# Performance work log

Measured on AMD Instinct MI355X. Metric: run time of the kernel, lower is better.

## Reference

```python
import jax, jax.numpy as jnp
import numpy as np
import math

# static config
NH, HD, HID = 16, 128, 2048
ROT = 64            # head_dim * partial_rotary_factor(0.5)
EPS = 1e-6
GROUPS = 8
CHUNK = 64
THETA = 10000.0
LAYER_IDX, N_LAYERS = 1, 32
B, S = 2, 2048


def _base_slopes(n):
    # power-of-two branch of HF ALiBi slopes
    start = 2 ** (-(2 ** (-(math.log2(n) - 3))))
    return [start * (start ** i) for i in range(n)]

# per-head log-decay (negative): slope = -base * (1 - (l-1)/(L-1) + 1e-5)
SLOPE = jnp.asarray(
    -np.array(_base_slopes(NH), dtype=np.float32)
    * (1.0 - (LAYER_IDX - 1) / (N_LAYERS - 1) + 1e-5),
    dtype=jnp.float32)  # [NH]


def _rmsnorm(x, w):
    return x * jax.lax.rsqrt(jnp.mean(x * x, axis=-1, keepdims=True) + EPS) * w


def _partial_rope(x, positions):
    # x: [B,S,NH,HD]; neox-style rotary on first ROT dims, rest passthrough
    half = ROT // 2
    inv_freq = 1.0 / (THETA ** (jnp.arange(half, dtype=jnp.float32) / half))
    ang = positions.astype(jnp.float32)[:, None] * inv_freq       # [S, half]
    cos = jnp.cos(ang)[None, :, None, :]
    sin = jnp.sin(ang)[None, :, None, :]
    x1, x2, rest = x[..., :half], x[..., half:ROT], x[..., ROT:]
    return jnp.concatenate(
        [x1 * cos - x2 * sin, x2 * cos + x1 * sin, rest], axis=-1)


def setup_inputs() -> dict:
    key = jax.random.key(0)
    ks = jax.random.split(key, 4)
    return {
        'positions': jnp.arange(S, dtype=jnp.int32),
        'hidden_states': jax.random.normal(ks[0], (B, S, HID), jnp.float32),
        'recurrent_state': jnp.zeros((B, NH, HD, HD), jnp.float32),
        'w_qkv': jax.random.normal(ks[1], (HID, 3 * NH * HD), jnp.float32) * 0.02,
        'w_g': jax.random.normal(ks[2], (HID, NH * HD), jnp.float32) * 0.02,
        'w_dense': jax.random.normal(ks[3], (NH * HD, HID), jnp.float32) * 0.02,
        'q_norm_w': jnp.ones((HD,), jnp.float32),
        'k_norm_w': jnp.ones((HD,), jnp.float32),
        'g_norm_w': jnp.ones((NH * HD,), jnp.float32),
    }


def reference(positions, hidden_states, recurrent_state, w_qkv, w_g, w_dense,
              q_norm_w, k_norm_w, g_norm_w):
    # fused QKV projection
    qkv = hidden_states @ w_qkv                       # [B,S,3*NH*HD]
    q, k, v = jnp.split(qkv, 3, axis=-1)
    q = q.reshape(B, S, NH, HD)
    k = k.reshape(B, S, NH, HD)
    v = v.reshape(B, S, NH, HD)

    # QK RMSNorm then partial rotary
    q = _partial_rope(_rmsnorm(q, q_norm_w), positions)
    k = _partial_rope(_rmsnorm(k, k_norm_w), positions)

    # chunked ALiBi-decayed linear attention:
    #   S_t = lam * S_{t-1} + k_t v_t^T ; o_t = q_t S_t, lam = exp(slope)
    NC = S // CHUNK
    qc = q.reshape(B, NC, CHUNK, NH, HD).transpose(1, 0, 3, 2, 4)  # [NC,B,NH,C,HD]
    kc = k.reshape(B, NC, CHUNK, NH, HD).transpose(1, 0, 3, 2, 4)
    vc = v.reshape(B, NC, CHUNK, NH, HD).transpose(1, 0, 3, 2, 4)

    t = jnp.arange(CHUNK, dtype=jnp.float32)
    # intra-chunk causal decay mask lam^(i-j), i>=j: [NH,C,C]
    dec_mask = jnp.where(t[:, None] >= t[None, :],
                         jnp.exp(SLOPE[:, None, None] * (t[:, None] - t[None, :])),
                         0.0)
    q_dec = jnp.exp(SLOPE[:, None] * (t[None, :] + 1.0))            # [NH,C] lam^(i+1)
    k_dec = jnp.exp(SLOPE[:, None] * (CHUNK - 1.0 - t[None, :]))    # [NH,C] lam^(C-1-j)
    lam_C = jnp.exp(SLOPE * CHUNK)                                   # [NH]

    def step(state, inp):
        qb, kb, vb = inp                                  # [B,NH,C,HD]
        scores = jnp.einsum('bhid,bhjd->bhij', qb, kb) * dec_mask[None]
        o_intra = jnp.einsum('bhij,bhjd->bhid', scores, vb)
        o_inter = jnp.einsum('bhid,bhde->bhie', qb * q_dec[None, :, :, None], state)
        new_state = (state * lam_C[None, :, None, None]
                     + jnp.einsum('bhjd,bhje->bhde', kb * k_dec[None, :, :, None], vb))
        return new_state, o_intra + o_inter

    _, o = jax.lax.scan(step, recurrent_state, (qc, kc, vc))  # o: [NC,B,NH,C,HD]
    o = o.transpose(1, 0, 3, 2, 4).reshape(B, S, NH * HD)

    # GroupRMSNorm on attention output, sigmoid gate, output projection
    og = o.reshape(B, S, GROUPS, (NH * HD) // GROUPS)
    og = og * jax.lax.rsqrt(jnp.mean(og * og, axis=-1, keepdims=True) + EPS)
    o = og.reshape(B, S, NH * HD) * g_norm_w
    o = o * jax.nn.sigmoid(hidden_states @ w_g)
    return o @ w_dense
```

## Files before the change

kernel.cpp:

```cpp
#include <hip/hip_runtime.h>
#include <hip/hip_bf16.h>
#include <math.h>

#define NH   16
#define HD   128
#define HID  2048
#define NKV  6144
#define B_   2
#define S_   2048
#define NC   32
#define CHUNK_ 64
#define GROUPS_ 8

typedef __bf16 bf16_t;
typedef bf16_t bf16x8 __attribute__((ext_vector_type(8)));
typedef float  f32x4  __attribute__((ext_vector_type(4)));

__device__ __forceinline__ float b2f(unsigned int u) {
    union { unsigned int u; float f; } c; c.u = (u & 0xffffu) << 16; return c.f;
}
__device__ __forceinline__ unsigned int f2b(float f) {
    union { float f; unsigned int u; } c; c.f = f;
    unsigned int u = c.u;
    return (u + 0x7fffu + ((u >> 16) & 1u)) >> 16;
}

#define GLOAD_LDS16(gp, lp) __builtin_amdgcn_global_load_lds(                     \
    (const __attribute__((address_space(1))) void*)(gp),                          \
    (__attribute__((address_space(3))) void*)(lp), 16, 0, 0)

#define BAR()     asm volatile("s_barrier" ::: "memory")
#define VMCNT0()  asm volatile("s_waitcnt vmcnt(0)" ::: "memory")

__global__ __launch_bounds__(256) void cvt_bf16(const float* __restrict__ in,
                                                unsigned short* __restrict__ out, int n8)
{
    int i = blockIdx.x * 256 + threadIdx.x;
    if (i >= n8) return;
    const float4* p = (const float4*)in + (size_t)i * 2;
    float4 a = p[0], b = p[1];
    uint4 o;
    o.x = f2b(a.x) | (f2b(a.y) << 16);
    o.y = f2b(a.z) | (f2b(a.w) << 16);
    o.z = f2b(b.x) | (f2b(b.y) << 16);
    o.w = f2b(b.z) | (f2b(b.w) << 16);
    ((uint4*)out)[i] = o;
}

__global__ __launch_bounds__(256) void transpose_cvt(const float* __restrict__ in,
                                                     unsigned short* __restrict__ out,
                                                     int Kdim, int Ndim)
{
    __shared__ float tile[32][33];
    int ntx = Ndim >> 5;
    int bx = blockIdx.x % ntx;
    int by = blockIdx.x / ntx;
    int lx = threadIdx.x & 31, ly = threadIdx.x >> 5;
    int r0 = by * 32, c0 = bx * 32;
    #pragma unroll
    for (int r = 0; r < 4; ++r)
        tile[ly + r * 8][lx] = in[(size_t)(r0 + ly + r * 8) * Ndim + c0 + lx];
    __syncthreads();
    #pragma unroll
    for (int r = 0; r < 4; ++r)
        out[(size_t)(c0 + ly + r * 8) * Kdim + r0 + lx] = (unsigned short)f2b(tile[lx][ly + r * 8]);
}

__global__ __launch_bounds__(256) void transpose_qg(const float* __restrict__ wq,
                                                    const float* __restrict__ wg,
                                                    unsigned short* __restrict__ out)
{
    __shared__ float tile[32][33];
    int bx = blockIdx.x & 255;
    int by = blockIdx.x >> 8;
    int lx = threadIdx.x & 31, ly = threadIdx.x >> 5;
    const float* in; int Ndim, c0;
    if (bx < 192) { in = wq; Ndim = NKV; c0 = bx * 32; }
    else          { in = wg; Ndim = HID; c0 = (bx - 192) * 32; }
    int r0 = by * 32;
    #pragma unroll
    for (int r = 0; r < 4; ++r)
        tile[ly + r * 8][lx] = in[(size_t)(r0 + ly + r * 8) * Ndim + c0 + lx];
    __syncthreads();
    #pragma unroll
    for (int r = 0; r < 4; ++r)
        out[(size_t)(bx * 32 + ly + r * 8) * HID + r0 + lx] = (unsigned short)f2b(tile[lx][ly + r * 8]);
}

__device__ __forceinline__ void ld_fr4(bf16x8 (&d)[4][2], const bf16_t* b, int s0, int ri) {
    #pragma unroll
    for (int i = 0; i < 4; ++i)
        #pragma unroll
        for (int k = 0; k < 2; ++k)
            d[i][k] = *(const bf16x8*)(b + (((s0 + i) * 2 + k) << 9) + ri);
}
__device__ __forceinline__ void ld_fr2(bf16x8 (&d)[2][2], const bf16_t* b, int s0, int ri) {
    #pragma unroll
    for (int i = 0; i < 2; ++i)
        #pragma unroll
        for (int k = 0; k < 2; ++k)
            d[i][k] = *(const bf16x8*)(b + (((s0 + i) * 2 + k) << 9) + ri);
}
__device__ __forceinline__ void mfma_quad(f32x4 (&a)[4][2], const bf16x8 (&af)[4][2],
                                          const bf16x8 (&bv)[2][2]) {
    #pragma unroll
    for (int mt = 0; mt < 4; ++mt)
        #pragma unroll
        for (int nt = 0; nt < 2; ++nt)
            #pragma unroll
            for (int ks = 0; ks < 2; ++ks)
                a[mt][nt] = __builtin_amdgcn_mfma_f32_16x16x32_bf16(af[mt][ks], bv[nt][ks], a[mt][nt], 0, 0, 0);
}

__global__ __launch_bounds__(512, 2) void gemm_qg_256(const bf16_t* __restrict__ A,
                                                      const bf16_t* __restrict__ Bt,
                                                      unsigned short* __restrict__ Cq,
                                                      unsigned short* __restrict__ Cg)
{
    __shared__ bf16_t Asm[2][2][8192];
    __shared__ bf16_t Bsm[2][2][8192];
    const int K  = HID;
    const int NT = K / 64;

    int tid  = threadIdx.x;
    int wave = tid >> 6, lane = tid & 63;
    int wm = wave >> 2, wn = wave & 3;
    int l16 = lane & 15, quad = lane >> 4;
    int wm4 = wm * 4, wn2 = wn * 2;

    int bid = blockIdx.x;
    int xcd = bid & 7, idx = bid >> 3;
    int by  = (xcd >> 2) * 8 + (idx >> 3);
    int bx  = (xcd & 3) * 8 + (idx & 7);

    int rd_in = ((l16 << 5) | (quad << 3)) ^ (((l16 >> 3) & 1) << 4);
    int ch = lane ^ ((lane & 32) >> 4);
    int rr = ch >> 2;
    int cc = (ch & 3) * 8;

    const bf16_t* aSrc0 = A  + (size_t)(by * 256 +       wave * 16 + rr) * K + cc;
    const bf16_t* aSrc1 = A  + (size_t)(by * 256 + 128 + wave * 16 + rr) * K + cc;
    const bf16_t* bSrc0 = Bt + (size_t)(bx * 256 +       wave * 16 + rr) * K + cc;
    const bf16_t* bSrc1 = Bt + (size_t)(bx * 256 + 128 + wave * 16 + rr) * K + cc;

#define STAGE_A(h, t) do {                                                        \
        const bf16_t* _g = ((h) ? aSrc1 : aSrc0) + (size_t)(t) * 64;              \
        bf16_t* _l = &Asm[(t) & 1][(h)][wave * 1024 + lane * 8];                  \
        GLOAD_LDS16(_g,      _l);                                                 \
        GLOAD_LDS16(_g + 32, _l + 512); } while (0)
#define STAGE_B(h, t) do {                                                        \
        const bf16_t* _g = ((h) ? bSrc1 : bSrc0) + (size_t)(t) * 64;              \
        bf16_t* _l = &Bsm[(t) & 1][(h)][wave * 1024 + lane * 8];                  \
        GLOAD_LDS16(_g,      _l);                                                 \
        GLOAD_LDS16(_g + 32, _l + 512); } while (0)

    f32x4 acc[2][2][4][2];
    #pragma unroll
    for (int a0 = 0; a0 < 2; ++a0)
        #pragma unroll
        for (int a1 = 0; a1 < 2; ++a1)
            #pragma unroll
            for (int a2 = 0; a2 < 4; ++a2)
                #pragma unroll
                for (int a3 = 0; a3 < 2; ++a3) { f32x4 z = {0.f,0.f,0.f,0.f}; acc[a0][a1][a2][a3] = z; }

    STAGE_A(0, 0); STAGE_B(0, 0); STAGE_A(1, 0); STAGE_B(1, 0);
    VMCNT0();
    BAR();

    #pragma unroll 2
    for (int t = 0; t < NT - 1; ++t) {
        const int buf = t & 1;
        STAGE_A(0, t + 1); STAGE_B(0, t + 1); STAGE_A(1, t + 1); STAGE_B(1, t + 1);
        {
            bf16x8 afA[4][2], afB[4][2], bf0[2][2], bf1[2][2];
            ld_fr4(afA, &Asm[buf][0][0], wm4, rd_in);
            ld_fr2(bf0, &Bsm[buf][0][0], wn2, rd_in);
            mfma_quad(acc[0][0], afA, bf0);
            ld_fr2(bf1, &Bsm[buf][1][0], wn2, rd_in);
            mfma_quad(acc[0][1], afA, bf1);
            ld_fr4(afB, &Asm[buf][1][0], wm4, rd_in);
            mfma_quad(acc[1][1], afB, bf1);
            mfma_quad(acc[1][0], afB, bf0);
        }
        VMCNT0();
        BAR();
    }
    {
        const int buf = (NT - 1) & 1;
        bf16x8 afA[4][2], afB[4][2], bf0[2][2], bf1[2][2];
        ld_fr4(afA, &Asm[buf][0][0], wm4, rd_in);
        ld_fr2(bf0, &Bsm[buf][0][0], wn2, rd_in);
        mfma_quad(acc[0][0], afA, bf0);
        ld_fr2(bf1, &Bsm[buf][1][0], wn2, rd_in);
        mfma_quad(acc[0][1], afA, bf1);
        ld_fr4(afB, &Asm[buf][1][0], wm4, rd_in);
        mfma_quad(acc[1][1], afB, bf1);
        mfma_quad(acc[1][0], afB, bf0);
    }
#undef STAGE_A
#undef STAGE_B

    unsigned short* Cc; int Nn, colbase;
    if (bx < 24) { Cc = Cq; Nn = NKV; colbase = bx * 256; }
    else         { Cc = Cg; Nn = HID; colbase = bx * 256 - NKV; }
    int row0 = by * 256 + wm * 64 + quad * 4;
    int col0 = colbase + wn * 32 + l16;
    #pragma unroll
    for (int mh = 0; mh < 2; ++mh)
        #pragma unroll
        for (int nh = 0; nh < 2; ++nh)
            #pragma unroll
            for (int mt = 0; mt < 4; ++mt)
                #pragma unroll
                for (int nt = 0; nt < 2; ++nt) {
                    int col = col0 + nh * 128 + nt * 16;
                    #pragma unroll
                    for (int r = 0; r < 4; ++r) {
                        int row = row0 + mh * 128 + mt * 16 + r;
                        Cc[(size_t)row * Nn + col] = (unsigned short)f2b(acc[mh][nh][mt][nt][r]);
                    }
                }
}

__global__ __launch_bounds__(256, 2) void gemm_out_128(const bf16_t* __restrict__ A,
                                                       const bf16_t* __restrict__ Bt,
                                                       float* __restrict__ C)
{
    __shared__ bf16_t As[2][4096];
    __shared__ bf16_t Bs[2][4096];
    const int K  = HID;
    const int NT = K / 32;

    int tid  = threadIdx.x;
    int wave = tid >> 6, lane = tid & 63;
    int wm2 = wave >> 1, wn2 = wave & 1;
    int l16 = lane & 15, quad = lane >> 4;
    int w2 = wave * 2;

    int bid = blockIdx.x;
    int xcd = bid & 7, idx = bid >> 3;
    int by  = (xcd >> 1) * 8 + (idx >> 3);
    int bx  = (xcd & 1) * 8 + (idx & 7);

    int rd_in = ((l16 << 5) | (quad << 3)) ^ (((l16 >> 3) & 1) << 4);
    int ch = lane ^ ((lane & 32) >> 4);
    int rr = ch >> 2;
    int cc = (ch & 3) * 8;

    const bf16_t* aSrc = A  + (size_t)(by * 128 + w2 * 16 + rr) * K + cc;
    const bf16_t* bSrc = Bt + (size_t)(bx * 128 + w2 * 16 + rr) * K + cc;

#define OSTAGE(t) do {                                                            \
        const int nb_ = (t) & 1;                                                  \
        const bf16_t* _ga = aSrc + (size_t)(t) * 32;                              \
        const bf16_t* _gb = bSrc + (size_t)(t) * 32;                              \
        GLOAD_LDS16(_ga,                  &As[nb_][w2 * 512 + lane * 8]);         \
        GLOAD_LDS16(_ga + (size_t)16 * K, &As[nb_][w2 * 512 + 512 + lane * 8]);   \
        GLOAD_LDS16(_gb,                  &Bs[nb_][w2 * 512 + lane * 8]);         \
        GLOAD_LDS16(_gb + (size_t)16 * K, &Bs[nb_][w2 * 512 + 512 + lane * 8]); } while (0)

    f32x4 acc[4][4];
    #pragma unroll
    for (int i = 0; i < 4; ++i)
        #pragma unroll
        for (int j = 0; j < 4; ++j) { f32x4 z = {0.f,0.f,0.f,0.f}; acc[i][j] = z; }

#define OCOMP(t) do {                                                             \
        const int b_ = (t) & 1;                                                   \
        bf16x8 af_[4], bf_[4];                                                    \
        _Pragma("unroll")                                                         \
        for (int i = 0; i < 4; ++i)                                               \
            af_[i] = *(const bf16x8*)(&As[b_][((wm2 * 4 + i) << 9) + rd_in]);     \
        _Pragma("unroll")                                                         \
        for (int j = 0; j < 4; ++j)                                               \
            bf_[j] = *(const bf16x8*)(&Bs[b_][((wn2 * 4 + j) << 9) + rd_in]);     \
        _Pragma("unroll")                                                         \
        for (int i = 0; i < 4; ++i)                                               \
            _Pragma("unroll")                                                     \
            for (int j = 0; j < 4; ++j)                                           \
                acc[i][j] = __builtin_amdgcn_mfma_f32_16x16x32_bf16(af_[i], bf_[j], acc[i][j], 0, 0, 0); } while (0)

    OSTAGE(0);
    VMCNT0();
    BAR();
    #pragma unroll 2
    for (int t = 0; t < NT - 1; ++t) {
        OSTAGE(t + 1);
        OCOMP(t);
        VMCNT0();
        BAR();
    }
    OCOMP(NT - 1);
#undef OSTAGE
#undef OCOMP

    #pragma unroll
    for (int i = 0; i < 4; ++i)
        #pragma unroll
        for (int j = 0; j < 4; ++j) {
            int col = bx * 128 + wn2 * 64 + j * 16 + l16;
            #pragma unroll
            for (int r = 0; r < 4; ++r) {
                int row = by * 128 + wm2 * 64 + i * 16 + quad * 4 + r;
                C[(size_t)row * HID + col] = acc[i][j][r];
            }
        }
}

__device__ __forceinline__ void nr_row(unsigned short* rowp, const float* __restrict__ w,
                                       float pos, int ln)
{
    uint4 v = *(const uint4*)(rowp + ln * 8);
    float x[8];
    x[0] = b2f(v.x); x[1] = b2f(v.x >> 16);
    x[2] = b2f(v.y); x[3] = b2f(v.y >> 16);
    x[4] = b2f(v.z); x[5] = b2f(v.z >> 16);
    x[6] = b2f(v.w); x[7] = b2f(v.w >> 16);
    float ss = 0.f;
    #pragma unroll
    for (int t = 0; t < 8; ++t) ss += x[t] * x[t];
    ss += __shfl_xor(ss, 1); ss += __shfl_xor(ss, 2);
    ss += __shfl_xor(ss, 4); ss += __shfl_xor(ss, 8);
    float inv = rsqrtf(ss * (1.0f / 128.0f) + 1e-6f);
    float n[8];
    #pragma unroll
    for (int t = 0; t < 8; ++t) n[t] = x[t] * inv * w[ln * 8 + t];
    float pr[8];
    #pragma unroll
    for (int t = 0; t < 8; ++t) pr[t] = __shfl_xor(n[t], 4);
    if (ln < 8) {
        #pragma unroll
        for (int t = 0; t < 8; ++t) {
            int dim = ln * 8 + t;
            int i = dim & 31;
            float ang = pos * exp2f(-(float)i * 0.4152410118609203f);
            float cs = cosf(ang), sn = sinf(ang);
            n[t] = (dim < 32) ? (n[t] * cs - pr[t] * sn) : (n[t] * cs + pr[t] * sn);
        }
    }
    uint4 o;
    o.x = f2b(n[0]) | (f2b(n[1]) << 16);
    o.y = f2b(n[2]) | (f2b(n[3]) << 16);
    o.z = f2b(n[4]) | (f2b(n[5]) << 16);
    o.w = f2b(n[6]) | (f2b(n[7]) << 16);
    *(uint4*)(rowp + ln * 8) = o;
}

__global__ __launch_bounds__(256) void chunk_kv(const unsigned short* __restrict__ qkv,
                                                const int* __restrict__ positions,
                                                const float* __restrict__ kw,
                                                unsigned short* __restrict__ wbuf)
{
    __shared__ unsigned short kraw[64 * 136];
    __shared__ unsigned short kt[128 * 72];
    __shared__ unsigned short vt[128 * 72];
    int bi = blockIdx.x;
    int c = bi & 31, bh = bi >> 5, h = bh & 15, b = bh >> 4;
    int tid = threadIdx.x;
    float slope = -exp2f(-0.5f * (float)(h + 1)) * (1.0f + 1e-5f);

    const unsigned short* kbase = qkv + ((size_t)(b * S_ + c * CHUNK_)) * NKV + HID + h * HD;
    const unsigned short* vbase = kbase + HID;

    for (int idx = tid; idx < 1024; idx += 256) {
        int row = idx >> 4, c8 = (idx & 15) * 8;
        *(uint4*)(kraw + row * 136 + c8) = *(const uint4*)(kbase + (size_t)row * NKV + c8);
    }
    for (int idx = tid; idx < 4096; idx += 256) {
        int j = idx >> 6, p = idx & 63;
        float kd = expf(slope * (float)(63 - j));
        unsigned int vu = *(const unsigned int*)(vbase + (size_t)j * NKV + p * 2);
        vt[(2 * p) * 72 + j]     = (unsigned short)f2b(b2f(vu) * kd);
        vt[(2 * p + 1) * 72 + j] = (unsigned short)f2b(b2f(vu >> 16) * kd);
    }
    __syncthreads();

    {
        int rp = tid >> 4, ln = tid & 15;
        #pragma unroll
        for (int pass = 0; pass < 4; ++pass) {
            int row = pass * 16 + rp;
            float pos = (float)positions[c * CHUNK_ + row];
            nr_row(kraw + row * 136, kw, pos, ln);
        }
    }
    __syncthreads();

    for (int idx = tid; idx < 4096; idx += 256) {
        int j = idx >> 6, p = idx & 63;
        unsigned int ku = *(const unsigned int*)(kraw + j * 136 + p * 2);
        kt[(2 * p) * 72 + j]     = (unsigned short)(ku & 0xffffu);
        kt[(2 * p + 1) * 72 + j] = (unsigned short)(ku >> 16);
    }
    __syncthreads();

    int lane = tid & 63, wave = tid >> 6;
    int wm = (wave >> 1) * 64;
    int wn = (wave & 1) * 64;
    int l16 = lane & 15, quad = lane >> 4;

    f32x4 acc[4][4];
    #pragma unroll
    for (int i = 0; i < 4; ++i)
        #pragma unroll
        for (int j = 0; j < 4; ++j) { f32x4 z = {0.f,0.f,0.f,0.f}; acc[i][j] = z; }

    #pragma unroll
    for (int ks = 0; ks < 64; ks += 32) {
        bf16x8 af[4], bf[4];
        #pragma unroll
        for (int t = 0; t < 4; ++t) {
            af[t] = *(const bf16x8*)((const bf16_t*)vt + (wm + t * 16 + l16) * 72 + ks + quad * 8);
            bf[t] = *(const bf16x8*)((const bf16_t*)kt + (wn + t * 16 + l16) * 72 + ks + quad * 8);
        }
        #pragma unroll
        for (int mt = 0; mt < 4; ++mt)
            #pragma unroll
            for (int nt = 0; nt < 4; ++nt)
                acc[mt][nt] = __builtin_amdgcn_mfma_f32_16x16x32_bf16(af[mt], bf[nt], acc[mt][nt], 0, 0, 0);
    }

    unsigned short* wp = wbuf + ((size_t)bi << 14);
    #pragma unroll
    for (int mt = 0; mt < 4; ++mt)
        #pragma unroll
        for (int nt = 0; nt < 4; ++nt) {
            int cid = ((wave >> 1) * 4 + mt) * 4 + (wave & 1) * 2 + (nt >> 1);
            int pos = ((nt & 1) * 2 + (l16 >> 3)) * 128 + (l16 & 7);
            #pragma unroll
            for (int r = 0; r < 4; ++r) {
                int e15 = quad * 4 + r;
                wp[cid * 512 + pos + e15 * 8] = (unsigned short)f2b(acc[mt][nt][r]);
            }
        }
}

__global__ __launch_bounds__(256) void state_scan(const unsigned short* __restrict__ wbuf,
                                                  const float* __restrict__ rs0,
                                                  unsigned short* __restrict__ stbuf)
{
    int bi = blockIdx.x;
    int s = bi & 7, bh = bi >> 3, h = bh & 15, b = bh >> 4;
    int tid = threadIdx.x;
    float slope = -exp2f(-0.5f * (float)(h + 1)) * (1.0f + 1e-5f);
    float lam = expf(slope * 64.0f);

    int T  = s * 256 + tid;
    int cid = T >> 6, lc = T & 63;
    int e  = (cid >> 2) * 16 + (lc & 15);
    int d0 = (cid & 3) * 32 + (lc >> 4) * 8;

    float S[8];
    const float* rp = rs0 + ((size_t)(b * NH + h)) * HD * HD + e;
    #pragma unroll
    for (int t = 0; t < 8; ++t) S[t] = rp[(size_t)(d0 + t) * HD];

    size_t base = (((size_t)bh * NC) << 14) + (size_t)T * 8;
    uint4 wr[4];
    #pragma unroll
    for (int i = 0; i < 4; ++i)
        wr[i] = *(const uint4*)(wbuf + base + ((size_t)i << 14));
    for (int c0 = 0; c0 < NC; c0 += 4) {
        #pragma unroll
        for (int u = 0; u < 4; ++u) {
            uint4 o;
            o.x = f2b(S[0]) | (f2b(S[1]) << 16);
            o.y = f2b(S[2]) | (f2b(S[3]) << 16);
            o.z = f2b(S[4]) | (f2b(S[5]) << 16);
            o.w = f2b(S[6]) | (f2b(S[7]) << 16);
            *(uint4*)(stbuf + base) = o;
            uint4 wc = wr[u];
            if (c0 + 4 + u < NC)
                wr[u] = *(const uint4*)(wbuf + base + ((size_t)4 << 14));
            S[0] = S[0] * lam + b2f(wc.x); S[1] = S[1] * lam + b2f(wc.x >> 16);
            S[2] = S[2] * lam + b2f(wc.y); S[3] = S[3] * lam + b2f(wc.y >> 16);
            S[4] = S[4] * lam + b2f(wc.z); S[5] = S[5] * lam + b2f(wc.z >> 16);
            S[6] = S[6] * lam + b2f(wc.w); S[7] = S[7] * lam + b2f(wc.w >> 16);
            base += (size_t)1 << 14;
        }
    }
}

__global__ __launch_bounds__(256) void chunk_out(const unsigned short* __restrict__ qkv,
                                                 const int* __restrict__ positions,
                                                 const float* __restrict__ qw,
                                                 const float* __restrict__ kw,
                                                 const unsigned short* __restrict__ stbuf,
                                                 unsigned short* __restrict__ obuf)
{
    __shared__ unsigned short qs[64 * 136];
    __shared__ unsigned short kss[64 * 136];
    __shared__ unsigned short vt[128 * 72];
    __shared__ unsigned short sc[64 * 72];

    int bi = blockIdx.x;
    int c = bi & 31, bh = bi >> 5, h = bh & 15, b = bh >> 4;
    int tid = threadIdx.x;
    float slope = -exp2f(-0.5f * (float)(h + 1)) * (1.0f + 1e-5f);

    int lane = tid & 63, wave = tid >> 6;
    int l16 = lane & 15, quad = lane >> 4;
    int wn3 = wave * 32;

    const unsigned short* stp = stbuf + (((size_t)bh * NC + c) << 14);
    bf16x8 bsf[4][2];
    #pragma unroll
    for (int ksp4 = 0; ksp4 < 4; ++ksp4)
        #pragma unroll
        for (int nt = 0; nt < 2; ++nt)
            bsf[ksp4][nt] = *(const bf16x8*)((const bf16_t*)stp +
                (((wave * 2 + nt) * 4 + ksp4) << 9) + lane * 8);

    const unsigned short* qrow = qkv + ((size_t)(b * S_ + c * CHUNK_)) * NKV + h * HD;
    const unsigned short* krow = qrow + HID;
    for (int idx = tid; idx < 1024; idx += 256) {
        int row = idx >> 4, c8 = (idx & 15) * 8;
        *(uint4*)(qs  + row * 136 + c8) = *(const uint4*)(qrow + (size_t)row * NKV + c8);
        *(uint4*)(kss + row * 136 + c8) = *(const uint4*)(krow + (size_t)row * NKV + c8);
    }
    const unsigned short* vbase = qrow + 2 * HID;
    for (int idx = tid; idx < 4096; idx += 256) {
        int j = idx >> 6, p = idx & 63;
        unsigned int vu = *(const unsigned int*)(vbase + (size_t)j * NKV + p * 2);
        vt[(2 * p) * 72 + j]     = (unsigned short)(vu & 0xffffu);
        vt[(2 * p + 1) * 72 + j] = (unsigned short)(vu >> 16);
    }
    __syncthreads();

    {
        int rp = tid >> 4, ln = tid & 15;
        #pragma unroll
        for (int pass = 0; pass < 4; ++pass) {
            int row = pass * 16 + rp;
            float pos = (float)positions[c * CHUNK_ + row];
            nr_row(qs  + row * 136, qw, pos, ln);
            nr_row(kss + row * 136, kw, pos, ln);
        }
    }
    __syncthreads();

    {
        f32x4 accS[4];
        #pragma unroll
        for (int t = 0; t < 4; ++t) { f32x4 z = {0.f,0.f,0.f,0.f}; accS[t] = z; }
        #pragma unroll
        for (int ksp = 0; ksp < 128; ksp += 32) {
            bf16x8 aq = *(const bf16x8*)((const bf16_t*)qs + (wave * 16 + l16) * 136 + ksp + quad * 8);
            #pragma unroll
            for (int nt = 0; nt < 4; ++nt) {
                bf16x8 bk = *(const bf16x8*)((const bf16_t*)kss + (nt * 16 + l16) * 136 + ksp + quad * 8);
                accS[nt] = __builtin_amdgcn_mfma_f32_16x16x32_bf16(aq, bk, accS[nt], 0, 0, 0);
            }
        }
        float ad[4];
        #pragma unroll
        for (int r = 0; r < 4; ++r) ad[r] = expf(slope * (float)(wave * 16 + quad * 4 + r));
        #pragma unroll
        for (int nt = 0; nt < 4; ++nt) {
            int j = nt * 16 + l16;
            float bd = expf(-slope * (float)j);
            #pragma unroll
            for (int r = 0; r < 4; ++r) {
                int i = wave * 16 + quad * 4 + r;
                float v = (i >= j) ? accS[nt][r] * ad[r] * bd : 0.0f;
                sc[i * 72 + j] = (unsigned short)f2b(v);
            }
        }
    }
    __syncthreads();

    f32x4 accI[4][2], accE[4][2];
    #pragma unroll
    for (int i = 0; i < 4; ++i)
        #pragma unroll
        for (int j = 0; j < 2; ++j) { f32x4 z = {0.f,0.f,0.f,0.f}; accI[i][j] = z; accE[i][j] = z; }

    #pragma unroll
    for (int ksp = 0; ksp < 64; ksp += 32) {
        bf16x8 as[4], bv[2];
        #pragma unroll
        for (int mt = 0; mt < 4; ++mt)
            as[mt] = *(const bf16x8*)((const bf16_t*)sc + (mt * 16 + l16) * 72 + ksp + quad * 8);
        #pragma unroll
        for (int nt = 0; nt < 2; ++nt)
            bv[nt] = *(const bf16x8*)((const bf16_t*)vt + (wn3 + nt * 16 + l16) * 72 + ksp + quad * 8);
        #pragma unroll
        for (int mt = 0; mt < 4; ++mt)
            #pragma unroll
            for (int nt = 0; nt < 2; ++nt)
                accI[mt][nt] = __builtin_amdgcn_mfma_f32_16x16x32_bf16(as[mt], bv[nt], accI[mt][nt], 0, 0, 0);
    }
    #pragma unroll
    for (int ksp4 = 0; ksp4 < 4; ++ksp4) {
        bf16x8 aq[4];
        #pragma unroll
        for (int mt = 0; mt < 4; ++mt)
            aq[mt] = *(const bf16x8*)((const bf16_t*)qs + (mt * 16 + l16) * 136 + ksp4 * 32 + quad * 8);
        #pragma unroll
        for (int mt = 0; mt < 4; ++mt)
            #pragma unroll
            for (int nt = 0; nt < 2; ++nt)
                accE[mt][nt] = __builtin_amdgcn_mfma_f32_16x16x32_bf16(aq[mt], bsf[ksp4][nt], accE[mt][nt], 0, 0, 0);
    }

    #pragma unroll
    for (int mt = 0; mt < 4; ++mt) {
        #pragma unroll
        for (int r = 0; r < 4; ++r) {
            int i = mt * 16 + quad * 4 + r;
            float qd = expf(slope * (float)(i + 1));
            int orow = b * S_ + c * CHUNK_ + i;
            #pragma unroll
            for (int nt = 0; nt < 2; ++nt) {
                int col = h * HD + wn3 + nt * 16 + l16;
                float o = accI[mt][nt][r] + qd * accE[mt][nt][r];
                obuf[(size_t)orow * 2048 + col] = (unsigned short)f2b(o);
            }
        }
    }
}

__global__ __launch_bounds__(256) void gnorm_gate(const unsigned short* __restrict__ o,
                                                  unsigned short* __restrict__ gate,
                                                  const float* __restrict__ gw)
{
    int row = blockIdx.x;
    int tid = threadIdx.x;
    size_t base8 = (size_t)row * 256 + tid;
    uint4 ov = ((const uint4*)o)[base8];
    uint4 gv = ((const uint4*)gate)[base8];
    float x[8];
    x[0] = b2f(ov.x); x[1] = b2f(ov.x >> 16);
    x[2] = b2f(ov.y); x[3] = b2f(ov.y >> 16);
    x[4] = b2f(ov.z); x[5] = b2f(ov.z >> 16);
    x[6] = b2f(ov.w); x[7] = b2f(ov.w >> 16);
    float ss = 0.f;
    #pragma unroll
    for (int t = 0; t < 8; ++t) ss += x[t] * x[t];
    ss += __shfl_xor(ss, 1); ss += __shfl_xor(ss, 2); ss += __shfl_xor(ss, 4);
    ss += __shfl_xor(ss, 8); ss += __shfl_xor(ss, 16);
    float inv = rsqrtf(ss * (1.0f / 256.0f) + 1e-6f);
    const float4* gwp = (const float4*)(gw + tid * 8);
    float4 w0 = gwp[0], w1 = gwp[1];
    float g[8];
    g[0] = b2f(gv.x); g[1] = b2f(gv.x >> 16);
    g[2] = b2f(gv.y); g[3] = b2f(gv.y >> 16);
    g[4] = b2f(gv.z); g[5] = b2f(gv.z >> 16);
    g[6] = b2f(gv.w); g[7] = b2f(gv.w >> 16);
    float wv[8] = {w0.x, w0.y, w0.z, w0.w, w1.x, w1.y, w1.z, w1.w};
    float r[8];
    #pragma unroll
    for (int t = 0; t < 8; ++t) {
        float sig = 1.0f / (1.0f + expf(-g[t]));
        r[t] = x[t] * inv * wv[t] * sig;
    }
    uint4 out;
    out.x = f2b(r[0]) | (f2b(r[1]) << 16);
    out.y = f2b(r[2]) | (f2b(r[3]) << 16);
    out.z = f2b(r[4]) | (f2b(r[5]) << 16);
    out.w = f2b(r[6]) | (f2b(r[7]) << 16);
    ((uint4*)gate)[base8] = out;
}

extern "C" void kernel_launch(void* const* d_in, const int* in_sizes, int n_in,
                              void* d_out, int out_size, void* d_ws, size_t ws_size,
                              hipStream_t stream) {
    const int*   positions = (const int*)d_in[0];
    const float* hidden    = (const float*)d_in[1];
    const float* rstate    = (const float*)d_in[2];
    const float* w_qkv     = (const float*)d_in[3];
    const float* w_g       = (const float*)d_in[4];
    const float* w_dense   = (const float*)d_in[5];
    const float* q_norm_w  = (const float*)d_in[6];
    const float* k_norm_w  = (const float*)d_in[7];
    const float* g_norm_w  = (const float*)d_in[8];
    float* out = (float*)d_out;

    const int MR = B_ * S_;

    char* w = (char*)d_ws;
    unsigned short* qkv  = (unsigned short*)w;            w += (size_t)MR * NKV * 2;
    unsigned short* gbuf = (unsigned short*)w;            w += (size_t)MR * 2048 * 2;
    unsigned short* wdT  = (unsigned short*)w;            w += (size_t)HID * HID * 2;
    char* regionA = w;                                    w += (size_t)MR * HID * 2 + (size_t)8192 * HID * 2;
    char* regionB = w;
    unsigned short* hbf   = (unsigned short*)regionA;
    unsigned short* btQG  = (unsigned short*)(regionA + (size_t)MR * HID * 2);
    unsigned short* stbuf = (unsigned short*)regionA;
    unsigned short* wbuf  = (unsigned short*)regionB;
    unsigned short* obuf  = (unsigned short*)regionB;

    cvt_bf16<<<dim3((MR * HID / 8 + 255) / 256), dim3(256), 0, stream>>>(hidden, hbf, MR * HID / 8);
    transpose_qg<<<dim3(64 * 256), dim3(256), 0, stream>>>(w_qkv, w_g, btQG);
    transpose_cvt<<<dim3((HID / 32) * (HID / 32)), dim3(256), 0, stream>>>(w_dense, wdT, HID, HID);

    gemm_qg_256<<<dim3(512), dim3(512), 0, stream>>>(
        (const bf16_t*)hbf, (const bf16_t*)btQG, qkv, gbuf);

    chunk_kv<<<dim3(B_ * NH * NC), dim3(256), 0, stream>>>(qkv, positions, k_norm_w, wbuf);
    state_scan<<<dim3(B_ * NH * 8), dim3(256), 0, stream>>>(wbuf, rstate, stbuf);
    chunk_out<<<dim3(B_ * NH * NC), dim3(256), 0, stream>>>(qkv, positions, q_norm_w, k_norm_w, stbuf, obuf);

    gnorm_gate<<<dim3(MR), dim3(256), 0, stream>>>(obuf, gbuf, g_norm_w);
    gemm_out_128<<<dim3(512), dim3(256), 0, stream>>>(
        (const bf16_t*)gbuf, (const bf16_t*)wdT, out);
}
```

Measured before the change: 473.4 us.

## Hoist q/k RMSNorm and RoPE into a standalone in-place kernel

Adds a norm_rope kernel that normalizes and rotates q and k in place in the qkv buffer once per token, instead of doing it inside both chunk_kv (k) and chunk_out (q and k). This removes duplicated k normalization, two shared-memory passes and barriers in chunk_kv, and one barrier in chunk_out. The cost is an extra launch and a full read/write pass over q and k in global memory. The state_scan prefetch is also changed from a 4-deep register ring to a 2-deep rolling prefetch.

Measured after the change: 421.8 us. 10.9% less time.

```diff
diff --git a/kernel.cpp b/kernel.cpp
--- a/kernel.cpp
+++ b/kernel.cpp
@@ -308,51 +308,65 @@
         }
 }
 
-__device__ __forceinline__ void nr_row(unsigned short* rowp, const float* __restrict__ w,
-                                       float pos, int ln)
-{
-    uint4 v = *(const uint4*)(rowp + ln * 8);
-    float x[8];
-    x[0] = b2f(v.x); x[1] = b2f(v.x >> 16);
-    x[2] = b2f(v.y); x[3] = b2f(v.y >> 16);
-    x[4] = b2f(v.z); x[5] = b2f(v.z >> 16);
-    x[6] = b2f(v.w); x[7] = b2f(v.w >> 16);
-    float ss = 0.f;
-    #pragma unroll
-    for (int t = 0; t < 8; ++t) ss += x[t] * x[t];
-    ss += __shfl_xor(ss, 1); ss += __shfl_xor(ss, 2);
-    ss += __shfl_xor(ss, 4); ss += __shfl_xor(ss, 8);
-    float inv = rsqrtf(ss * (1.0f / 128.0f) + 1e-6f);
-    float n[8];
-    #pragma unroll
-    for (int t = 0; t < 8; ++t) n[t] = x[t] * inv * w[ln * 8 + t];
-    float pr[8];
-    #pragma unroll
-    for (int t = 0; t < 8; ++t) pr[t] = __shfl_xor(n[t], 4);
-    if (ln < 8) {
-        #pragma unroll
-        for (int t = 0; t < 8; ++t) {
-            int dim = ln * 8 + t;
-            int i = dim & 31;
-            float ang = pos * exp2f(-(float)i * 0.4152410118609203f);
-            float cs = cosf(ang), sn = sinf(ang);
-            n[t] = (dim < 32) ? (n[t] * cs - pr[t] * sn) : (n[t] * cs + pr[t] * sn);
-        }
-    }
-    uint4 o;
-    o.x = f2b(n[0]) | (f2b(n[1]) << 16);
-    o.y = f2b(n[2]) | (f2b(n[3]) << 16);
-    o.z = f2b(n[4]) | (f2b(n[5]) << 16);
-    o.w = f2b(n[6]) | (f2b(n[7]) << 16);
-    *(uint4*)(rowp + ln * 8) = o;
+__global__ __launch_bounds__(256) void norm_rope(unsigned short* __restrict__ qkv,
+                                                 const int* __restrict__ positions,
+                                                 const float* __restrict__ qw,
+                                                 const float* __restrict__ kw)
+{
+    int bs = blockIdx.x;
+    int s  = bs & (S_ - 1);
+    int tid = threadIdx.x;
+    int l16 = tid & 15;
+    unsigned short* base = qkv + (size_t)bs * NKV;
+    float pos = (float)positions[s];
+
+    #pragma unroll
+    for (int p = 0; p < 2; ++p) {
+        int rr = p * 16 + (tid >> 4);
+        int qk = rr >> 4;
+        int h  = rr & 15;
+        unsigned short* row = base + qk * HID + h * HD;
+        const float* w = qk ? kw : qw;
+        uint4 v = *(const uint4*)(row + l16 * 8);
+        float x[8];
+        x[0] = b2f(v.x); x[1] = b2f(v.x >> 16);
+        x[2] = b2f(v.y); x[3] = b2f(v.y >> 16);
+        x[4] = b2f(v.z); x[5] = b2f(v.z >> 16);
+        x[6] = b2f(v.w); x[7] = b2f(v.w >> 16);
+        float ss = 0.f;
+        #pragma unroll
+        for (int t = 0; t < 8; ++t) ss += x[t] * x[t];
+        ss += __shfl_xor(ss, 1); ss += __shfl_xor(ss, 2);
+        ss += __shfl_xor(ss, 4); ss += __shfl_xor(ss, 8);
+        float inv = rsqrtf(ss * (1.0f / 128.0f) + 1e-6f);
+        float n[8];
+        #pragma unroll
+        for (int t = 0; t < 8; ++t) n[t] = x[t] * inv * w[l16 * 8 + t];
+        float pr[8];
+        #pragma unroll
+        for (int t = 0; t < 8; ++t) pr[t] = __shfl_xor(n[t], 4);
+        if (l16 < 8) {
+            #pragma unroll
+            for (int t = 0; t < 8; ++t) {
+                int dim = l16 * 8 + t;
+                int i = dim & 31;
+                float ang = pos * exp2f(-(float)i * 0.4152410118609203f);
+                float cs = cosf(ang), sn = sinf(ang);
+                n[t] = (dim < 32) ? (n[t] * cs - pr[t] * sn) : (n[t] * cs + pr[t] * sn);
+            }
+        }
+        uint4 o;
+        o.x = f2b(n[0]) | (f2b(n[1]) << 16);
+        o.y = f2b(n[2]) | (f2b(n[3]) << 16);
+        o.z = f2b(n[4]) | (f2b(n[5]) << 16);
+        o.w = f2b(n[6]) | (f2b(n[7]) << 16);
+        *(uint4*)(row + l16 * 8) = o;
+    }
 }
 
 __global__ __launch_bounds__(256) void chunk_kv(const unsigned short* __restrict__ qkv,
-                                                const int* __restrict__ positions,
-                                                const float* __restrict__ kw,
                                                 unsigned short* __restrict__ wbuf)
 {
-    __shared__ unsigned short kraw[64 * 136];
     __shared__ unsigned short kt[128 * 72];
     __shared__ unsigned short vt[128 * 72];
     int bi = blockIdx.x;
@@ -363,35 +377,15 @@
     const unsigned short* kbase = qkv + ((size_t)(b * S_ + c * CHUNK_)) * NKV + HID + h * HD;
     const unsigned short* vbase = kbase + HID;
 
-    for (int idx = tid; idx < 1024; idx += 256) {
-        int row = idx >> 4, c8 = (idx & 15) * 8;
-        *(uint4*)(kraw + row * 136 + c8) = *(const uint4*)(kbase + (size_t)row * NKV + c8);
-    }
     for (int idx = tid; idx < 4096; idx += 256) {
         int j = idx >> 6, p = idx & 63;
+        unsigned int ku = *(const unsigned int*)(kbase + (size_t)j * NKV + p * 2);
+        kt[(2 * p) * 72 + j]     = (unsigned short)(ku & 0xffffu);
+        kt[(2 * p + 1) * 72 + j] = (unsigned short)(ku >> 16);
         float kd = expf(slope * (float)(63 - j));
         unsigned int vu = *(const unsigned int*)(vbase + (size_t)j * NKV + p * 2);
         vt[(2 * p) * 72 + j]     = (unsigned short)f2b(b2f(vu) * kd);
         vt[(2 * p + 1) * 72 + j] = (unsigned short)f2b(b2f(vu >> 16) * kd);
-    }
-    __syncthreads();
-
-    {
-        int rp = tid >> 4, ln = tid & 15;
-        #pragma unroll
-        for (int pass = 0; pass < 4; ++pass) {
-            int row = pass * 16 + rp;
-            float pos = (float)positions[c * CHUNK_ + row];
-            nr_row(kraw + row * 136, kw, pos, ln);
-        }
-    }
-    __syncthreads();
-
-    for (int idx = tid; idx < 4096; idx += 256) {
-        int j = idx >> 6, p = idx & 63;
-        unsigned int ku = *(const unsigned int*)(kraw + j * 136 + p * 2);
-        kt[(2 * p) * 72 + j]     = (unsigned short)(ku & 0xffffu);
-        kt[(2 * p + 1) * 72 + j] = (unsigned short)(ku >> 16);
     }
     __syncthreads();
 
@@ -457,35 +451,27 @@
     for (int t = 0; t < 8; ++t) S[t] = rp[(size_t)(d0 + t) * HD];
 
     size_t base = (((size_t)bh * NC) << 14) + (size_t)T * 8;
-    uint4 wr[4];
-    #pragma unroll
-    for (int i = 0; i < 4; ++i)
-        wr[i] = *(const uint4*)(wbuf + base + ((size_t)i << 14));
-    for (int c0 = 0; c0 < NC; c0 += 4) {
-        #pragma unroll
-        for (int u = 0; u < 4; ++u) {
-            uint4 o;
-            o.x = f2b(S[0]) | (f2b(S[1]) << 16);
-            o.y = f2b(S[2]) | (f2b(S[3]) << 16);
-            o.z = f2b(S[4]) | (f2b(S[5]) << 16);
-            o.w = f2b(S[6]) | (f2b(S[7]) << 16);
-            *(uint4*)(stbuf + base) = o;
-            uint4 wc = wr[u];
-            if (c0 + 4 + u < NC)
-                wr[u] = *(const uint4*)(wbuf + base + ((size_t)4 << 14));
-            S[0] = S[0] * lam + b2f(wc.x); S[1] = S[1] * lam + b2f(wc.x >> 16);
-            S[2] = S[2] * lam + b2f(wc.y); S[3] = S[3] * lam + b2f(wc.y >> 16);
-            S[4] = S[4] * lam + b2f(wc.z); S[5] = S[5] * lam + b2f(wc.z >> 16);
-            S[6] = S[6] * lam + b2f(wc.w); S[7] = S[7] * lam + b2f(wc.w >> 16);
-            base += (size_t)1 << 14;
-        }
+    uint4 w0 = *(const uint4*)(wbuf + base);
+    uint4 w1 = *(const uint4*)(wbuf + base + (1 << 14));
+    for (int c = 0; c < NC; ++c) {
+        uint4 o;
+        o.x = f2b(S[0]) | (f2b(S[1]) << 16);
+        o.y = f2b(S[2]) | (f2b(S[3]) << 16);
+        o.z = f2b(S[4]) | (f2b(S[5]) << 16);
+        o.w = f2b(S[6]) | (f2b(S[7]) << 16);
+        *(uint4*)(stbuf + base) = o;
+        uint4 w2 = w1;
+        if (c + 2 < NC) w2 = *(const uint4*)(wbuf + base + (2 << 14));
+        S[0] = S[0] * lam + b2f(w0.x); S[1] = S[1] * lam + b2f(w0.x >> 16);
+        S[2] = S[2] * lam + b2f(w0.y); S[3] = S[3] * lam + b2f(w0.y >> 16);
+        S[4] = S[4] * lam + b2f(w0.z); S[5] = S[5] * lam + b2f(w0.z >> 16);
+        S[6] = S[6] * lam + b2f(w0.w); S[7] = S[7] * lam + b2f(w0.w >> 16);
+        w0 = w1; w1 = w2;
+        base += (1 << 14);
     }
 }
 
 __global__ __launch_bounds__(256) void chunk_out(const unsigned short* __restrict__ qkv,
-                                                 const int* __restrict__ positions,
-                                                 const float* __restrict__ qw,
-                                                 const float* __restrict__ kw,
                                                  const unsigned short* __restrict__ stbuf,
                                                  unsigned short* __restrict__ obuf)
 {
@@ -525,18 +511,6 @@
         unsigned int vu = *(const unsigned int*)(vbase + (size_t)j * NKV + p * 2);
         vt[(2 * p) * 72 + j]     = (unsigned short)(vu & 0xffffu);
         vt[(2 * p + 1) * 72 + j] = (unsigned short)(vu >> 16);
-    }
-    __syncthreads();
-
-    {
-        int rp = tid >> 4, ln = tid & 15;
-        #pragma unroll
-        for (int pass = 0; pass < 4; ++pass) {
-            int row = pass * 16 + rp;
-            float pos = (float)positions[c * CHUNK_ + row];
-            nr_row(qs  + row * 136, qw, pos, ln);
-            nr_row(kss + row * 136, kw, pos, ln);
-        }
     }
     __syncthreads();
 
@@ -697,10 +671,11 @@
 
     gemm_qg_256<<<dim3(512), dim3(512), 0, stream>>>(
         (const bf16_t*)hbf, (const bf16_t*)btQG, qkv, gbuf);
-
-    chunk_kv<<<dim3(B_ * NH * NC), dim3(256), 0, stream>>>(qkv, positions, k_norm_w, wbuf);
+    norm_rope<<<dim3(B_ * S_), dim3(256), 0, stream>>>(qkv, positions, q_norm_w, k_norm_w);
+
+    chunk_kv<<<dim3(B_ * NH * NC), dim3(256), 0, stream>>>(qkv, wbuf);
     state_scan<<<dim3(B_ * NH * 8), dim3(256), 0, stream>>>(wbuf, rstate, stbuf);
-    chunk_out<<<dim3(B_ * NH * NC), dim3(256), 0, stream>>>(qkv, positions, q_norm_w, k_norm_w, stbuf, obuf);
+    chunk_out<<<dim3(B_ * NH * NC), dim3(256), 0, stream>>>(qkv, stbuf, obuf);
 
     gnorm_gate<<<dim3(MR), dim3(256), 0, stream>>>(obuf, gbuf, g_norm_w);
     gemm_out_128<<<dim3(512), dim3(256), 0, stream>>>(
```
